# Kernel tuning notes

Hardware: AMD Instinct MI355X
Metric: run time of the kernel (lower is better)

Reference implementation:

```python
import jax, jax.numpy as jnp
import numpy as np

EMBED_DIM = 300
HIDDEN = 128
N_CLS = 20
N_NODES = 100000
N_EDGES = 1600000
N_GRAPHS = 512
EPSILON = 1e-06


def setup_inputs() -> dict:
    key = jax.random.key(0)
    ks = jax.random.split(key, 10)
    x_fp16 = jax.random.normal(ks[0], (N_NODES, EMBED_DIM), dtype=jnp.float16)
    ei = jax.random.randint(ks[1], (2, N_EDGES), 0, N_NODES, dtype=jnp.int32)
    batch = jnp.sort(jax.random.randint(ks[2], (N_NODES,), 0, N_GRAPHS, dtype=jnp.int32))
    mask = jax.random.randint(ks[3], (N_NODES,), 0, 2, dtype=jnp.int32).astype(jnp.bool_)
    def glorot(k, fan_in, fan_out):
        s = (6.0 / (fan_in + fan_out)) ** 0.5
        return jax.random.uniform(k, (fan_in, fan_out), jnp.float32, -s, s)
    return {
        "x_fp16": x_fp16, "ei": ei, "batch": batch, "mask": mask,
        "W1": glorot(ks[4], EMBED_DIM, HIDDEN), "b1": jnp.zeros((HIDDEN,), jnp.float32),
        "W2": glorot(ks[5], HIDDEN, HIDDEN), "b2": jnp.zeros((HIDDEN,), jnp.float32),
        "Wout": glorot(ks[6], HIDDEN, N_CLS), "bout": jnp.zeros((N_CLS,), jnp.float32),
    }


def gcn_conv(x, W, b, src, dst, n):
    # PyG GCNConv: x' = D^{-1/2} (A + I) D^{-1/2} (x W) + b
    h = x @ W  # [N, out]
    loop = jnp.arange(n, dtype=src.dtype)
    s = jnp.concatenate([src, loop])
    d = jnp.concatenate([dst, loop])
    deg = jax.ops.segment_sum(jnp.ones_like(d, dtype=h.dtype), d, num_segments=n)
    dinv = jax.lax.rsqrt(deg)  # deg >= 1 thanks to self-loops
    norm = dinv[s] * dinv[d]  # [E+N]
    msg = h[s] * norm[:, None]
    return jax.ops.segment_sum(msg, d, num_segments=n) + b


def reference(x_fp16, ei, batch, mask, W1, b1, W2, b2, Wout, bout):
    n = x_fp16.shape[0]
    src, dst = ei[0], ei[1]
    x = x_fp16.astype(jnp.float32)
    x = jax.nn.relu(gcn_conv(x, W1, b1, src, dst, n))
    x = jax.nn.relu(gcn_conv(x, W2, b2, src, dst, n))
    m = mask.astype(jnp.float32)[:, None]  # [N,1]
    ent_sum = jax.ops.segment_sum(x * m, batch, num_segments=N_GRAPHS)  # [G,H]
    ent_cnt = jax.ops.segment_sum(m, batch, num_segments=N_GRAPHS)  # [G,1]
    doc_vec = ent_sum / (ent_cnt + EPSILON)
    # fallback: mean over all nodes when a graph has no masked entities
    node_sum = jax.ops.segment_sum(x, batch, num_segments=N_GRAPHS)
    node_cnt = jax.ops.segment_sum(jnp.ones((n, 1), jnp.float32), batch, num_segments=N_GRAPHS)
    mean_pool = node_sum / jnp.maximum(node_cnt, 1.0)
    zero = ent_cnt < EPSILON  # [G,1]
    doc_vec = jnp.where(zero, mean_pool, doc_vec)
    return jax.nn.log_softmax(doc_vec @ Wout + bout, axis=1)
```

## Files before the change

kernel.cpp:

```cpp
#include <hip/hip_runtime.h>
#include <hip/hip_fp16.h>

#define NN 100000
#define NE 1600000
#define DIM 300
#define HID 128
#define NC 20
#define NG 512
#define NBK 196
#define BCH 4096

typedef _Float16 h8 __attribute__((ext_vector_type(8)));
typedef float f4 __attribute__((ext_vector_type(4)));

union pack16 { float4 v; __half2 h2[4]; };

__device__ __forceinline__ __half tohalf(float v) {
  if (!(v == v)) v = 0.f;
  v = fminf(fmaxf(v, -60000.f), 60000.f);
  return __float2half(v);
}

__device__ __forceinline__ float load_x(const void* xraw, size_t o, int mode) {
  float v;
  if (mode == 2) v = ((const float*)xraw)[o];
  else {
    unsigned short u = ((const unsigned short*)xraw)[o];
    if (mode == 1) { union { unsigned w; float f; } c; c.w = ((unsigned)u) << 16; v = c.f; }
    else { union { unsigned short s; _Float16 h; } c; c.s = u; v = (float)c.h; }
  }
  if (!(v == v)) v = 0.f;
  return fminf(fmaxf(v, -1e4f), 1e4f);
}

__device__ __forceinline__ void cvt4(const void* Ain, size_t off, int mode, _Float16* o) {
  if (mode == 2) {
    float4 fv = *(const float4*)((const float*)Ain + off);
    o[0] = (_Float16)fv.x; o[1] = (_Float16)fv.y; o[2] = (_Float16)fv.z; o[3] = (_Float16)fv.w;
  } else {
    uint2 u = *(const uint2*)((const unsigned short*)Ain + off);
    unsigned short s0 = u.x & 0xFFFF, s1 = u.x >> 16, s2 = u.y & 0xFFFF, s3 = u.y >> 16;
    if (mode == 1) {
      union { unsigned w; float f; } c0, c1, c2, c3;
      c0.w = ((unsigned)s0) << 16; c1.w = ((unsigned)s1) << 16;
      c2.w = ((unsigned)s2) << 16; c3.w = ((unsigned)s3) << 16;
      o[0] = (_Float16)c0.f; o[1] = (_Float16)c1.f; o[2] = (_Float16)c2.f; o[3] = (_Float16)c3.f;
    } else {
      union { unsigned short s; _Float16 h; } d0, d1, d2, d3;
      d0.s = s0; d1.s = s1; d2.s = s2; d3.s = s3;
      o[0] = d0.h; o[1] = d1.h; o[2] = d2.h; o[3] = d3.h;
    }
  }
}


__global__ void k_probe(const unsigned short* __restrict__ xu,
                        const unsigned* __restrict__ Araw, const unsigned* __restrict__ Braw,
                        const int* __restrict__ e32,
                        const float* __restrict__ W1, const float* __restrict__ W2,
                        _Float16* __restrict__ w1f, _Float16* __restrict__ w2f,
                        unsigned* __restrict__ diag) {
  int b = blockIdx.x, t = threadIdx.x;
  if (b < 96) {
    int mode = b % 3, chunk = b / 3;
    float m = 0.f;
    if (mode == 0) {
      int base = chunk * 16384;
      for (int j = t; j < 16384; j += 256) {
        union { unsigned short s; _Float16 h; } c; c.s = xu[base + j];
        float v = fabsf((float)c.h);
        if (v == v && v < 65000.f) m = fmaxf(m, v);
      }
    } else if (mode == 1) {
      int base = chunk * 16384;
      for (int j = t; j < 16384; j += 256) {
        union { unsigned w; float f; } c; c.w = ((unsigned)xu[base + j]) << 16;
        float v = fabsf(c.f);
        if (v == v && v < 1e30f) m = fmaxf(m, v);
      }
    } else {
      const float* xf = (const float*)xu;
      int base = chunk * 8192;
      for (int j = t; j < 8192; j += 256) {
        float v = fabsf(xf[base + j]);
        if (v == v && v < 1e30f) m = fmaxf(m, v);
      }
    }
    for (int off = 32; off; off >>= 1) m = fmaxf(m, __shfl_xor(m, off));
    if ((t & 63) == 0) atomicMax(&diag[20 + mode], __float_as_uint(m));
  } else if (b == 96 || b == 97) {
    __shared__ unsigned red[256];
    const unsigned* p = (b == 96) ? Araw : Braw;
    unsigned m = 0;
    for (int j = t; j < 25000; j += 256) m = max(m, p[j]);
    red[t] = m; __syncthreads();
    for (int off = 128; off; off >>= 1) { if (t < off) red[t] = max(red[t], red[t + off]); __syncthreads(); }
    if (t == 0) diag[(b == 96) ? 24 : 25] = red[0];
  } else if (b < 102) {
    int i = (b - 98) * 256 + t;
    unsigned z = 0;
    for (; i < 50000; i += 1024) if (e32[2 * i + 1] == 0) z++;
    for (int off = 32; off; off >>= 1) z += __shfl_xor(z, off);
    if ((t & 63) == 0) atomicAdd(&diag[26], z);
  } else {
    int idx = (b - 102) * 256 + t;
    const int S1 = 10 * 8 * 64 * 8;
    const int S2 = 4 * 8 * 64 * 8;
    if (idx < S1) {
      int j = idx & 7, l = (idx >> 3) & 63, nt = (idx >> 9) & 7, kc = idx >> 12;
      int k = kc * 32 + ((l >> 4) << 3) + j;
      int n = nt * 16 + (l & 15);
      w1f[idx] = (k < DIM) ? (_Float16)W1[k * HID + n] : (_Float16)0.f;
    } else if (idx < S1 + S2) {
      int q = idx - S1;
      int j = q & 7, l = (q >> 3) & 63, nt = (q >> 9) & 7, kc = q >> 12;
      int k = kc * 32 + ((l >> 4) << 3) + j;
      int n = nt * 16 + (l & 15);
      w2f[q] = (_Float16)W2[k * HID + n];
    }
  }
}


__global__ void k_setup(const unsigned* __restrict__ diag, int* __restrict__ flags,
                        const int* __restrict__ A, const int* __restrict__ B,
                        int* __restrict__ bcnt, int* __restrict__ gstart) {
  __shared__ int sflags[8];
  int t = threadIdx.x;
  if (t == 0) {
    float M16 = __uint_as_float(diag[20]);
    float M32 = __uint_as_float(diag[21]);
    float Mf  = __uint_as_float(diag[22]);
    int xmode = 3;
    if      (Mf  > 3.f && Mf  < 8.f) xmode = 2;
    else if (M32 > 3.f && M32 < 8.f) xmode = 1;
    else if (M16 > 3.f && M16 < 8.f) xmode = 0;
    unsigned uA = diag[24], uB = diag[25];
    bool Ab = (uA >= 32u && uA < 1024u), Bb = (uB >= 32u && uB < 1024u);
    int swap = -1;
    if (Ab && !Bb) swap = 0;
    else if (Bb && !Ab) swap = 1;
    int mint = -1;
    if (swap >= 0) {
      unsigned um = (swap == 0) ? uB : uA;
      if (um <= 1u) mint = 1;
      else if (um >= 65536u) mint = 0;
    }
    sflags[0] = xmode;
    sflags[1] = (mint == 1) ? 1 : 0;
    sflags[2] = (swap == 1) ? 1 : 0;
    sflags[3] = (diag[26] >= 49990u) ? 1 : 0;
    sflags[4] = (swap >= 0 && mint >= 0) ? 1 : 0;
    #pragma unroll
    for (int j = 0; j < 5; j++) flags[j] = sflags[j];
  }
  __syncthreads();
  const int* batch = sflags[2] ? B : A;
  if (t <= NG) {
    if (t == NG) gstart[NG] = NN;
    else {
      int lo = 0, hi = NN;
      while (lo < hi) { int mid = (lo + hi) >> 1; if (batch[mid] < t) lo = mid + 1; else hi = mid; }
      gstart[t] = lo;
    }
  }
  if (t < NBK) bcnt[t] = 0;
}


__global__ void k_bhist(const int* __restrict__ e32, const int* __restrict__ flags,
                        int* __restrict__ bcnt, int* __restrict__ boff,
                        int* __restrict__ bcur, unsigned* __restrict__ done) {
  __shared__ int hist[NBK];
  int e64 = flags[3];
  int t = threadIdx.x;
  for (int j = t; j < NBK; j += 256) hist[j] = 0;
  __syncthreads();
  int i = blockIdx.x * blockDim.x + t;
  int stride = gridDim.x * blockDim.x;
  for (; i < NE; i += stride) {
    int s = e64 ? e32[2 * i] : e32[i];
    int d = e64 ? e32[2 * NE + 2 * i] : e32[NE + i];
    if ((unsigned)s < (unsigned)NN && (unsigned)d < (unsigned)NN)
      atomicAdd(&hist[d >> 9], 1);
  }
  __syncthreads();
  for (int j = t; j < NBK; j += 256) if (hist[j]) atomicAdd(&bcnt[j], hist[j]);
  __threadfence();
  __syncthreads();
  if (t == 0) {
    if (atomicAdd(done, 1u) == gridDim.x - 1) {
      int run = 0;
      for (int j = 0; j < NBK; j++) { boff[j] = run; bcur[j] = run; run += bcnt[j]; }
      boff[NBK] = run;
    }
  }
}

__global__ __launch_bounds__(256)
void k_bscatter(const int* __restrict__ e32, const int* __restrict__ flags,
                int* __restrict__ bcur, unsigned* __restrict__ ebuf) {
  __shared__ uint2 stage[BCH];
  __shared__ int hist[NBK];
  __shared__ int lbase[NBK];
  __shared__ int lcur[NBK];
  int e64 = flags[3];
  int t = threadIdx.x;
  for (int j = t; j < NBK; j += 256) { hist[j] = 0; lcur[j] = 0; }
  __syncthreads();
  int start = blockIdx.x * BCH;
  int n = NE - start; if (n > BCH) n = BCH;
  for (int i = t; i < n; i += 256) {
    int idx = start + i;
    int s = e64 ? e32[2 * idx] : e32[idx];
    int d = e64 ? e32[2 * NE + 2 * idx] : e32[NE + idx];
    bool ok = ((unsigned)s < (unsigned)NN) && ((unsigned)d < (unsigned)NN);
    stage[i] = make_uint2(ok ? (unsigned)s : 0xFFFFFFFFu, (unsigned)(ok ? d : 0));
    if (ok) atomicAdd(&hist[d >> 9], 1);
  }
  __syncthreads();
  for (int j = t; j < NBK; j += 256) if (hist[j] > 0) lbase[j] = atomicAdd(&bcur[j], hist[j]);
  __syncthreads();
  for (int i = t; i < n; i += 256) {
    unsigned s = stage[i].x;
    if (s == 0xFFFFFFFFu) continue;
    int d = (int)stage[i].y;
    int b = d >> 9;
    int o = atomicAdd(&lcur[b], 1);
    ebuf[lbase[b] + o] = (s << 9) | (unsigned)(d & 511);
  }
}

__global__ __launch_bounds__(256)
void k_bfinal(const unsigned* __restrict__ ebuf, const int* __restrict__ boff,
              int* __restrict__ row_off, float* __restrict__ dinv, int* __restrict__ csr) {
  __shared__ int ldeg[512];
  __shared__ int lcur[512];
  int b = blockIdx.x, t = threadIdx.x;
  int base = b * 512;
  int nn = NN - base; if (nn > 512) nn = 512;
  for (int j = t; j < 512; j += 256) ldeg[j] = 0;
  __syncthreads();
  int s0 = boff[b], s1 = boff[b + 1];
  for (int e = s0 + t; e < s1; e += 256) atomicAdd(&ldeg[ebuf[e] & 511], 1);
  __syncthreads();
  if (t == 0) {
    int run = s0;
    for (int i = 0; i < nn; i++) { lcur[i] = run; row_off[base + i] = run; run += ldeg[i]; }
    if (b == gridDim.x - 1) row_off[NN] = run;
  }
  __syncthreads();
  for (int j = t; j < nn; j += 256) dinv[base + j] = rsqrtf((float)ldeg[j] + 1.0f);
  for (int e = s0 + t; e < s1; e += 256) {
    unsigned v = ebuf[e];
    int p = atomicAdd(&lcur[v & 511], 1);
    csr[p] = (int)(v >> 9);
  }
}


#define XS1 168

__global__ __launch_bounds__(512)
void k_gemm1_mfma(const void* __restrict__ Ain, const _Float16* __restrict__ bfrag,
                  const float* __restrict__ dinv, const int* __restrict__ flags,
                  __half* __restrict__ outg) {
  __shared__ _Float16 xs[64 * XS1];
  const int mode = flags[0] & 3;
  int tid = threadIdx.x;
  int w = tid >> 6, l = tid & 63;
  int rowbase = blockIdx.x * 64;
  int k0base = (l >> 4) << 3;
  int cb = l & 15;

  f4 acc[4];
  f4 zero = {0.f, 0.f, 0.f, 0.f};
  #pragma unroll
  for (int rg = 0; rg < 4; rg++) acc[rg] = zero;

  #pragma unroll
  for (int it = 0; it < 5; it++) {
    int c = tid + it * 512;
    int rl = c / 40, kk = (c - rl * 40) * 4;
    int r = rowbase + rl;
    _Float16 o[4] = {0, 0, 0, 0};
    if (r < NN) cvt4(Ain, (size_t)r * DIM + kk, mode, o);
    _Float16* p = &xs[rl * XS1 + kk];
    p[0] = o[0]; p[1] = o[1]; p[2] = o[2]; p[3] = o[3];
  }
  __syncthreads();
  #pragma unroll
  for (int kc = 0; kc < 5; kc++) {
    int ko = kc * 32 + k0base;
    h8 a0 = *(const h8*)&xs[(0 * 16 + cb) * XS1 + ko];
    h8 a1 = *(const h8*)&xs[(1 * 16 + cb) * XS1 + ko];
    h8 a2 = *(const h8*)&xs[(2 * 16 + cb) * XS1 + ko];
    h8 a3 = *(const h8*)&xs[(3 * 16 + cb) * XS1 + ko];
    h8 bv = *(const h8*)&bfrag[(((kc << 3) + w) * 64 + l) * 8];
    acc[0] = __builtin_amdgcn_mfma_f32_16x16x32_f16(a0, bv, acc[0], 0, 0, 0);
    acc[1] = __builtin_amdgcn_mfma_f32_16x16x32_f16(a1, bv, acc[1], 0, 0, 0);
    acc[2] = __builtin_amdgcn_mfma_f32_16x16x32_f16(a2, bv, acc[2], 0, 0, 0);
    acc[3] = __builtin_amdgcn_mfma_f32_16x16x32_f16(a3, bv, acc[3], 0, 0, 0);
  }
  __syncthreads();

  for (int t2 = tid; t2 < 64 * 10; t2 += 512) {
    int rl = t2 / 10, j = t2 - rl * 10;
    *(unsigned*)&xs[rl * XS1 + 140 + j * 2] = 0u;
  }
  #pragma unroll
  for (int it = 0; it < 5; it++) {
    int c = tid + it * 512;
    if (c < 64 * 35) {
      int rl = c / 35, kk = (c - rl * 35) * 4;
      int r = rowbase + rl;
      _Float16 o[4] = {0, 0, 0, 0};
      if (r < NN) cvt4(Ain, (size_t)r * DIM + 160 + kk, mode, o);
      _Float16* p = &xs[rl * XS1 + kk];
      p[0] = o[0]; p[1] = o[1]; p[2] = o[2]; p[3] = o[3];
    }
  }
  __syncthreads();
  #pragma unroll
  for (int kc = 5; kc < 10; kc++) {
    int ko = (kc - 5) * 32 + k0base;
    h8 a0 = *(const h8*)&xs[(0 * 16 + cb) * XS1 + ko];
    h8 a1 = *(const h8*)&xs[(1 * 16 + cb) * XS1 + ko];
    h8 a2 = *(const h8*)&xs[(2 * 16 + cb) * XS1 + ko];
    h8 a3 = *(const h8*)&xs[(3 * 16 + cb) * XS1 + ko];
    h8 bv = *(const h8*)&bfrag[(((kc << 3) + w) * 64 + l) * 8];
    acc[0] = __builtin_amdgcn_mfma_f32_16x16x32_f16(a0, bv, acc[0], 0, 0, 0);
    acc[1] = __builtin_amdgcn_mfma_f32_16x16x32_f16(a1, bv, acc[1], 0, 0, 0);
    acc[2] = __builtin_amdgcn_mfma_f32_16x16x32_f16(a2, bv, acc[2], 0, 0, 0);
    acc[3] = __builtin_amdgcn_mfma_f32_16x16x32_f16(a3, bv, acc[3], 0, 0, 0);
  }

  int rquad = (l >> 4) << 2;
  #pragma unroll
  for (int rg = 0; rg < 4; rg++) {
    #pragma unroll
    for (int i = 0; i < 4; i++) {
      int r = rowbase + rg * 16 + rquad + i;
      if (r >= NN) continue;
      float dv = dinv[r];
      outg[(size_t)r * HID + w * 16 + cb] = tohalf(acc[rg][i] * dv);
    }
  }
}


__global__ __launch_bounds__(256)
void k_gemm2_mfma(const __half* __restrict__ Ain, const _Float16* __restrict__ bfrag,
                  const float* __restrict__ dinv, __half* __restrict__ outg) {
  __shared__ _Float16 xs[64 * 136];
  int tid = threadIdx.x;
  int w = tid >> 6, l = tid & 63;
  int rowbase = blockIdx.x * 64;
  int k0base = (l >> 4) << 3;
  int cb = l & 15;

  {
    h8 regs[4];
    #pragma unroll
    for (int it = 0; it < 4; it++) {
      int c = tid + it * 256;
      int rl = c >> 4, k = (c & 15) * 8;
      int r = rowbase + rl;
      h8 v = {};
      if (r < NN) v = *(const h8*)((const _Float16*)Ain + (size_t)r * HID + k);
      regs[it] = v;
    }
    __builtin_amdgcn_sched_barrier(0);
    #pragma unroll
    for (int it = 0; it < 4; it++) {
      int c = tid + it * 256;
      int rl = c >> 4, k = (c & 15) * 8;
      *(h8*)&xs[rl * 136 + k] = regs[it];
    }
  }
  __syncthreads();

  f4 acc[4][2];
  f4 zero = {0.f, 0.f, 0.f, 0.f};
  #pragma unroll
  for (int rg = 0; rg < 4; rg++) { acc[rg][0] = zero; acc[rg][1] = zero; }

  #pragma unroll
  for (int kc = 0; kc < 4; kc++) {
    int ko = kc * 32 + k0base;
    h8 a0 = *(const h8*)&xs[(0 * 16 + cb) * 136 + ko];
    h8 a1 = *(const h8*)&xs[(1 * 16 + cb) * 136 + ko];
    h8 a2 = *(const h8*)&xs[(2 * 16 + cb) * 136 + ko];
    h8 a3 = *(const h8*)&xs[(3 * 16 + cb) * 136 + ko];
    #pragma unroll
    for (int ntl = 0; ntl < 2; ntl++) {
      int nt = w * 2 + ntl;
      h8 bv = *(const h8*)&bfrag[(((kc << 3) + nt) * 64 + l) * 8];
      acc[0][ntl] = __builtin_amdgcn_mfma_f32_16x16x32_f16(a0, bv, acc[0][ntl], 0, 0, 0);
      acc[1][ntl] = __builtin_amdgcn_mfma_f32_16x16x32_f16(a1, bv, acc[1][ntl], 0, 0, 0);
      acc[2][ntl] = __builtin_amdgcn_mfma_f32_16x16x32_f16(a2, bv, acc[2][ntl], 0, 0, 0);
      acc[3][ntl] = __builtin_amdgcn_mfma_f32_16x16x32_f16(a3, bv, acc[3][ntl], 0, 0, 0);
    }
  }

  int rquad = (l >> 4) << 2;
  #pragma unroll
  for (int rg = 0; rg < 4; rg++) {
    #pragma unroll
    for (int i = 0; i < 4; i++) {
      int r = rowbase + rg * 16 + rquad + i;
      if (r >= NN) continue;
      float dv = dinv[r];
      __half* orow = outg + (size_t)r * HID;
      orow[(w * 2 + 0) * 16 + cb] = tohalf(acc[rg][0][i] * dv);
      orow[(w * 2 + 1) * 16 + cb] = tohalf(acc[rg][1][i] * dv);
    }
  }
}


__global__ __launch_bounds__(256)
void k_agg(const __half* __restrict__ g, const float* __restrict__ dinv,
           const int* __restrict__ row_off, const int* __restrict__ csr,
           const float* __restrict__ bias, __half* __restrict__ out) {
  int tid = threadIdx.x;
  int node = blockIdx.x * 4 + (tid >> 6);
  int l = tid & 63;
  if (node >= NN) return;
  int grp = l >> 4;
  int cl  = l & 15;
  size_t coff = (size_t)cl * 8;

  float a0 = 0.f, a1 = 0.f, a2 = 0.f, a3 = 0.f, a4 = 0.f, a5 = 0.f, a6 = 0.f, a7 = 0.f;
  pack16 r;

  #define ACCUM() do { \
    float2 f0 = __half22float2(r.h2[0]); \
    float2 f1 = __half22float2(r.h2[1]); \
    float2 f2 = __half22float2(r.h2[2]); \
    float2 f3 = __half22float2(r.h2[3]); \
    a0 += f0.x; a1 += f0.y; a2 += f1.x; a3 += f1.y; \
    a4 += f2.x; a5 += f2.y; a6 += f3.x; a7 += f3.y; } while (0)

  int e0 = row_off[node], e1 = row_off[node + 1];
  int e = e0 + grp;
  for (; e + 4 < e1; e += 8) {
    int s1 = csr[e], s2 = csr[e + 4];
    pack16 rA, rB;
    rA.v = *(const float4*)(g + (size_t)s1 * HID + coff);
    rB.v = *(const float4*)(g + (size_t)s2 * HID + coff);
    r = rA; ACCUM();
    r = rB; ACCUM();
  }
  if (e < e1) {
    int s1 = csr[e];
    r.v = *(const float4*)(g + (size_t)s1 * HID + coff);
    ACCUM();
  }
  if (grp == 0) {
    r.v = *(const float4*)(g + (size_t)node * HID + coff);
    ACCUM();
  }
  #undef ACCUM

  a0 += __shfl_xor(a0, 16); a1 += __shfl_xor(a1, 16); a2 += __shfl_xor(a2, 16); a3 += __shfl_xor(a3, 16);
  a4 += __shfl_xor(a4, 16); a5 += __shfl_xor(a5, 16); a6 += __shfl_xor(a6, 16); a7 += __shfl_xor(a7, 16);
  a0 += __shfl_xor(a0, 32); a1 += __shfl_xor(a1, 32); a2 += __shfl_xor(a2, 32); a3 += __shfl_xor(a3, 32);
  a4 += __shfl_xor(a4, 32); a5 += __shfl_xor(a5, 32); a6 += __shfl_xor(a6, 32); a7 += __shfl_xor(a7, 32);

  if (grp == 0) {
    float di = dinv[node];
    const float* bp = bias + coff;
    pack16 w;
    w.h2[0] = __floats2half2_rn(fmaxf(a0 * di + bp[0], 0.f), fmaxf(a1 * di + bp[1], 0.f));
    w.h2[1] = __floats2half2_rn(fmaxf(a2 * di + bp[2], 0.f), fmaxf(a3 * di + bp[3], 0.f));
    w.h2[2] = __floats2half2_rn(fmaxf(a4 * di + bp[4], 0.f), fmaxf(a5 * di + bp[5], 0.f));
    w.h2[3] = __floats2half2_rn(fmaxf(a6 * di + bp[6], 0.f), fmaxf(a7 * di + bp[7], 0.f));
    *(float4*)(out + (size_t)node * HID + coff) = w.v;
  }
}


__global__ __launch_bounds__(256)
void k_pool(const __half* __restrict__ o2, const void* __restrict__ Araw, const void* __restrict__ Braw,
            const int* __restrict__ gstart, const int* __restrict__ flags,
            const float* __restrict__ Wout, const float* __restrict__ bout,
            float* __restrict__ out) {
  __shared__ float lex[4][HID];
  __shared__ float lnx[4][HID];
  __shared__ int lec[4];
  __shared__ float ldoc[HID];
  int gid = blockIdx.x, tid = threadIdx.x;
  int wv = tid >> 6, l = tid & 63;
  int grp = l >> 4, cl = l & 15;
  size_t coff = (size_t)cl * 8;
  const int mint = flags[1];
  const void* mraw = flags[2] ? Araw : Braw;
  const unsigned char* m8 = (const unsigned char*)mraw;
  const int* m32 = (const int*)mraw;
  int s = gstart[gid], e = gstart[gid + 1];

  float ex[8], nx[8];
  #pragma unroll
  for (int j = 0; j < 8; j++) { ex[j] = 0.f; nx[j] = 0.f; }
  int ec = 0;

  for (int n = s + wv * 4 + grp; n < e; n += 16) {
    pack16 r;
    r.v = *(const float4*)(o2 + (size_t)n * HID + coff);
    float2 f0 = __half22float2(r.h2[0]);
    float2 f1 = __half22float2(r.h2[1]);
    float2 f2 = __half22float2(r.h2[2]);
    float2 f3 = __half22float2(r.h2[3]);
    float t0 = f0.x, t1 = f0.y, t2 = f1.x, t3 = f1.y;
    float t4 = f2.x, t5 = f2.y, t6 = f3.x, t7 = f3.y;
    nx[0] += t0; nx[1] += t1; nx[2] += t2; nx[3] += t3;
    nx[4] += t4; nx[5] += t5; nx[6] += t6; nx[7] += t7;
    bool mv = mint ? (m32[n] != 0) : (m8[n] != 0);
    if (mv) {
      ex[0] += t0; ex[1] += t1; ex[2] += t2; ex[3] += t3;
      ex[4] += t4; ex[5] += t5; ex[6] += t6; ex[7] += t7;
      ec++;
    }
  }
  #pragma unroll
  for (int j = 0; j < 8; j++) {
    ex[j] += __shfl_xor(ex[j], 16); ex[j] += __shfl_xor(ex[j], 32);
    nx[j] += __shfl_xor(nx[j], 16); nx[j] += __shfl_xor(nx[j], 32);
  }
  ec += __shfl_xor(ec, 16); ec += __shfl_xor(ec, 32);

  if (grp == 0) {
    #pragma unroll
    for (int j = 0; j < 8; j++) { lex[wv][cl * 8 + j] = ex[j]; lnx[wv][cl * 8 + j] = nx[j]; }
    if (cl == 0) lec[wv] = ec;
  }
  __syncthreads();
  if (tid < HID) {
    float exT = lex[0][tid] + lex[1][tid] + lex[2][tid] + lex[3][tid];
    float nxT = lnx[0][tid] + lnx[1][tid] + lnx[2][tid] + lnx[3][tid];
    int ecT = lec[0] + lec[1] + lec[2] + lec[3];
    int cnt = e - s;
    float dv;
    if (ecT > 0) dv = exT / ((float)ecT + 1e-6f);
    else dv = (cnt > 0) ? nxT / (float)cnt : 0.f;
    ldoc[tid] = dv;
  }
  __syncthreads();
  if (tid < 64) {
    float logit = -1e30f;
    if (tid < NC) {
      float acc = bout[tid];
      for (int k = 0; k < HID; k++) acc += ldoc[k] * Wout[k * NC + tid];
      logit = acc;
    }
    float m = logit;
    for (int off = 32; off; off >>= 1) m = fmaxf(m, __shfl_xor(m, off));
    float exv = (tid < NC) ? expf(logit - m) : 0.f;
    float ssum = exv;
    for (int off = 32; off; off >>= 1) ssum += __shfl_xor(ssum, off);
    if (tid < NC) out[gid * NC + tid] = (logit - m) - logf(ssum);
  }
}

__global__ void k_fail(float* __restrict__ out, float enc) {
  int i = blockIdx.x * blockDim.x + threadIdx.x;
  if (i < NG * NC) out[i] = -enc;
}


extern "C" void kernel_launch(void* const* d_in, const int* in_sizes, int n_in,
                              void* d_out, int out_size, void* d_ws, size_t ws_size,
                              hipStream_t stream) {
  int ix = -1, iei = -1, iA = -1, iB = -1, iW1 = -1, ib1 = -1, iW2 = -1, ib2 = -1, iWo = -1, ibo = -1;
  for (int i = 0; i < n_in; i++) {
    int s = in_sizes[i];
    if (s == 30000000) ix = i;
    else if (s == 3200000) iei = i;
    else if (s == 100000) { if (iA < 0) iA = i; else iB = i; }
    else if (s == 38400) iW1 = i;
    else if (s == 16384) iW2 = i;
    else if (s == 2560) iWo = i;
    else if (s == 20) ibo = i;
    else if (s == 128) { if (ib1 < 0) ib1 = i; else ib2 = i; }
  }
  float* out = (float*)d_out;
  int miss = -1;
  if (ix < 0) miss = 0; else if (iei < 0) miss = 1; else if (iA < 0 || iB < 0) miss = 2;
  else if (iW1 < 0) miss = 3; else if (ib1 < 0 || ib2 < 0) miss = 4; else if (iW2 < 0) miss = 5;
  else if (iWo < 0) miss = 6; else if (ibo < 0) miss = 7;
  if (miss >= 0) {
    k_fail<<<(NG * NC + 255) / 256, 256, 0, stream>>>(out, 8192.f + 64.f * (float)miss);
    return;
  }
  const void* x = d_in[ix];
  const int* e32 = (const int*)d_in[iei];
  const void* Araw = d_in[iA];
  const void* Braw = d_in[iB];
  const float* W1 = (const float*)d_in[iW1];
  const float* b1 = (const float*)d_in[ib1];
  const float* W2 = (const float*)d_in[iW2];
  const float* b2 = (const float*)d_in[ib2];
  const float* Wout = (const float*)d_in[iWo];
  const float* bout = (const float*)d_in[ibo];

  char* ws = (char*)d_ws;
  size_t off = 0;
  auto alloc = [&](size_t bytes) -> char* {
    char* p = ws + off; off += (bytes + 255) & ~(size_t)255; return p;
  };
  float* dinv   = (float*)alloc((size_t)NN * 4);
  int* row_off  = (int*)alloc((size_t)(NN + 1) * 4);
  int* csr      = (int*)alloc((size_t)NE * 4);
  int* bcnt     = (int*)alloc((size_t)NBK * 4);
  int* boff     = (int*)alloc((size_t)(NBK + 1) * 4);
  int* bcur     = (int*)alloc((size_t)NBK * 4);
  int* gstart   = (int*)alloc((size_t)(NG + 1) * 4);
  int* flags    = (int*)alloc(8 * 4);
  _Float16* w1f = (_Float16*)alloc(40960 * 2);
  _Float16* w2f = (_Float16*)alloc(16384 * 2);
  __half* gbuf  = (__half*)alloc((size_t)NN * HID * 2);
  __half* obuf  = (__half*)alloc((size_t)NN * HID * 2);
  float* doc    = (float*)alloc((size_t)NG * HID * 4);
  unsigned* diag = (unsigned*)alloc(64 * 4);
  unsigned* ebuf = (unsigned*)gbuf;

  hipMemsetAsync(diag, 0, 64 * 4, stream);

  k_probe<<<326, 256, 0, stream>>>((const unsigned short*)x, (const unsigned*)Araw,
                                   (const unsigned*)Braw, e32, W1, W2, w1f, w2f, diag);
  k_setup<<<1, 576, 0, stream>>>(diag, flags, (const int*)Araw, (const int*)Braw, bcnt, gstart);

  k_bhist<<<1024, 256, 0, stream>>>(e32, flags, bcnt, boff, bcur, &diag[32]);
  k_bscatter<<<(NE + BCH - 1) / BCH, 256, 0, stream>>>(e32, flags, bcur, ebuf);
  k_bfinal<<<NBK, 256, 0, stream>>>(ebuf, boff, row_off, dinv, csr);

  k_gemm1_mfma<<<(NN + 63) / 64, 512, 0, stream>>>(x, w1f, dinv, flags, gbuf);
  k_agg<<<NN / 4, 256, 0, stream>>>(gbuf, dinv, row_off, csr, b1, obuf);
  k_gemm2_mfma<<<(NN + 63) / 64, 256, 0, stream>>>(obuf, w2f, dinv, gbuf);
  k_agg<<<NN / 4, 256, 0, stream>>>(gbuf, dinv, row_off, csr, b2, obuf);

  k_pool<<<NG, 256, 0, stream>>>(obuf, Araw, Braw, gstart, flags, Wout, bout, out);
}
```

Baseline: 344.8 us.

## Replace atomic bucket histogram with per-block histograms and a scan kernel

The bucket histogram no longer uses global atomics and a last-block-done counter. Each of 256 blocks now writes its own row of per-bucket counts, and a new single-block kernel sums the rows and builds the prefix offsets. The scatter chunk size doubles to 8192 edges, which halves the scatter grid and doubles its shared-memory staging. The changes trade global atomic contention and the threadfence for one extra kernel launch, and larger scatter blocks may lower occupancy.

After: 297.0 us. 1.16x faster.

```diff
diff --git a/kernel.cpp b/kernel.cpp
--- a/kernel.cpp
+++ b/kernel.cpp
@@ -8,7 +8,8 @@
 #define NC 20
 #define NG 512
 #define NBK 196
-#define BCH 4096
+#define BCH 8192
+#define NHB 256
 
 typedef _Float16 h8 __attribute__((ext_vector_type(8)));
 typedef float f4 __attribute__((ext_vector_type(4)));
@@ -124,7 +125,7 @@
 
 __global__ void k_setup(const unsigned* __restrict__ diag, int* __restrict__ flags,
                         const int* __restrict__ A, const int* __restrict__ B,
-                        int* __restrict__ bcnt, int* __restrict__ gstart) {
+                        int* __restrict__ gstart) {
   __shared__ int sflags[8];
   int t = threadIdx.x;
   if (t == 0) {
@@ -164,19 +165,18 @@
       gstart[t] = lo;
     }
   }
-  if (t < NBK) bcnt[t] = 0;
-}
-
-
-__global__ void k_bhist(const int* __restrict__ e32, const int* __restrict__ flags,
-                        int* __restrict__ bcnt, int* __restrict__ boff,
-                        int* __restrict__ bcur, unsigned* __restrict__ done) {
+}
+
+
+__global__ __launch_bounds__(256)
+void k_bhist(const int* __restrict__ e32, const int* __restrict__ flags,
+             int* __restrict__ hist2d) {
   __shared__ int hist[NBK];
   int e64 = flags[3];
-  int t = threadIdx.x;
+  int b = blockIdx.x, t = threadIdx.x;
   for (int j = t; j < NBK; j += 256) hist[j] = 0;
   __syncthreads();
-  int i = blockIdx.x * blockDim.x + t;
+  int i = b * blockDim.x + t;
   int stride = gridDim.x * blockDim.x;
   for (; i < NE; i += stride) {
     int s = e64 ? e32[2 * i] : e32[i];
@@ -185,15 +185,23 @@
       atomicAdd(&hist[d >> 9], 1);
   }
   __syncthreads();
-  for (int j = t; j < NBK; j += 256) if (hist[j]) atomicAdd(&bcnt[j], hist[j]);
-  __threadfence();
+  for (int j = t; j < NBK; j += 256) hist2d[b * NBK + j] = hist[j];
+}
+
+__global__ __launch_bounds__(256)
+void k_bscan(const int* __restrict__ hist2d, int* __restrict__ boff, int* __restrict__ bcur) {
+  __shared__ int sums[NBK];
+  int t = threadIdx.x;
+  if (t < NBK) {
+    int s = 0;
+    for (int b = 0; b < NHB; b++) s += hist2d[b * NBK + t];
+    sums[t] = s;
+  }
   __syncthreads();
   if (t == 0) {
-    if (atomicAdd(done, 1u) == gridDim.x - 1) {
-      int run = 0;
-      for (int j = 0; j < NBK; j++) { boff[j] = run; bcur[j] = run; run += bcnt[j]; }
-      boff[NBK] = run;
-    }
+    int run = 0;
+    for (int j = 0; j < NBK; j++) { boff[j] = run; bcur[j] = run; run += sums[j]; }
+    boff[NBK] = run;
   }
 }
 
@@ -612,7 +620,7 @@
   float* dinv   = (float*)alloc((size_t)NN * 4);
   int* row_off  = (int*)alloc((size_t)(NN + 1) * 4);
   int* csr      = (int*)alloc((size_t)NE * 4);
-  int* bcnt     = (int*)alloc((size_t)NBK * 4);
+  int* hist2d   = (int*)alloc((size_t)NHB * NBK * 4);
   int* boff     = (int*)alloc((size_t)(NBK + 1) * 4);
   int* bcur     = (int*)alloc((size_t)NBK * 4);
   int* gstart   = (int*)alloc((size_t)(NG + 1) * 4);
@@ -621,7 +629,6 @@
   _Float16* w2f = (_Float16*)alloc(16384 * 2);
   __half* gbuf  = (__half*)alloc((size_t)NN * HID * 2);
   __half* obuf  = (__half*)alloc((size_t)NN * HID * 2);
-  float* doc    = (float*)alloc((size_t)NG * HID * 4);
   unsigned* diag = (unsigned*)alloc(64 * 4);
   unsigned* ebuf = (unsigned*)gbuf;
 
@@ -629,9 +636,10 @@
 
   k_probe<<<326, 256, 0, stream>>>((const unsigned short*)x, (const unsigned*)Araw,
                                    (const unsigned*)Braw, e32, W1, W2, w1f, w2f, diag);
-  k_setup<<<1, 576, 0, stream>>>(diag, flags, (const int*)Araw, (const int*)Braw, bcnt, gstart);
-
-  k_bhist<<<1024, 256, 0, stream>>>(e32, flags, bcnt, boff, bcur, &diag[32]);
+  k_setup<<<1, 576, 0, stream>>>(diag, flags, (const int*)Araw, (const int*)Braw, gstart);
+
+  k_bhist<<<NHB, 256, 0, stream>>>(e32, flags, hist2d);
+  k_bscan<<<1, 256, 0, stream>>>(hist2d, boff, bcur);
   k_bscatter<<<(NE + BCH - 1) / BCH, 256, 0, stream>>>(e32, flags, bcur, ebuf);
   k_bfinal<<<NBK, 256, 0, stream>>>(ebuf, boff, row_off, dinv, csr);
 
```
